# Kernel optimization log

Hardware: AMD Instinct MI355X
Metric: run time of the kernel (lower is better)

## Reference

```python
import jax, jax.numpy as jnp
import numpy as np

B, N, CIN, COUT, K, L, NNZ = 4, 4096, 128, 128, 10, 50, 65536


def _spmm(idx, vals, X):
    # COO spmm: out[r] += vals * X[c]; idx: [2, nnz], X: [N, F]
    rows, cols = idx[0], idx[1]
    return jax.ops.segment_sum(vals[:, None] * X[cols], rows, num_segments=N)

_bspmm = jax.vmap(_spmm, in_axes=(0, 0, 0))  # batched over leading dim


def _hgnn_layer(phi_idx, phi_val, inv_idx, inv_val, fea, W, d):
    # original: ((phi @ diag(d)) @ phi_inv) @ (fea @ W)
    # identical math, evaluated right-to-left to stay sparse-dense only
    filt = jnp.einsum('bnc,co->bno', fea, W)            # [B,N,COUT]
    y = _bspmm(inv_idx, inv_val, filt)                  # phi_inv @ X
    y = d[None, :, None] * y                            # diag(d) @ .
    return _bspmm(phi_idx, phi_val, y)                  # phi @ .


def setup_inputs() -> dict:
    key = jax.random.key(0)
    ks = jax.random.split(key, 20)

    def coo(ki, kv):
        idx = jax.random.randint(ki, (B, 2, NNZ), 0, N, dtype=jnp.int32)
        val = jax.random.normal(kv, (B, NNZ), jnp.float32) * 0.05
        return idx, val

    phi1_idx, phi1_val = coo(ks[0], ks[1])
    phi1_inv_idx, phi1_inv_val = coo(ks[2], ks[3])
    phi2_idx, phi2_val = coo(ks[4], ks[5])
    phi2_inv_idx, phi2_inv_val = coo(ks[6], ks[7])
    fea = jax.random.normal(ks[8], (B, N, CIN), jnp.float32)
    joblst = jax.random.randint(ks[9], (B, L), 0, N, dtype=jnp.int64)

    xavier = float(np.sqrt(6.0 / (CIN + COUT)))
    W1 = jax.random.uniform(ks[10], (CIN, COUT), jnp.float32, -xavier, xavier)
    W2 = jax.random.uniform(ks[11], (CIN, COUT), jnp.float32, -xavier, xavier)
    d1 = jax.random.uniform(ks[12], (N,), jnp.float32, 0.9, 1.1)
    d2 = jax.random.uniform(ks[13], (N,), jnp.float32, 0.9, 1.1)
    s = float(1.0 / np.sqrt(N))
    W_ih = jax.random.uniform(ks[14], (N, COUT), jnp.float32, -s, s)
    W_hh = jax.random.uniform(ks[15], (N, N), jnp.float32, -s, s)
    b_ih = jax.random.uniform(ks[16], (N,), jnp.float32, -s, s)
    b_hh = jnp.zeros((N,), jnp.float32)
    sd = float(1.0 / np.sqrt(COUT))
    dense_W = jax.random.uniform(ks[17], (K, COUT), jnp.float32, -sd, sd)
    dense_b = jnp.zeros((K,), jnp.float32)
    item_emb = jax.random.normal(ks[18], (N, COUT), jnp.float32) * 0.01

    return dict(phi1_idx=phi1_idx, phi1_val=phi1_val, phi1_inv_idx=phi1_inv_idx,
                phi1_inv_val=phi1_inv_val, phi2_idx=phi2_idx, phi2_val=phi2_val,
                phi2_inv_idx=phi2_inv_idx, phi2_inv_val=phi2_inv_val,
                fea=fea, joblst=joblst, W1=W1, d1=d1, W2=W2, d2=d2,
                W_ih=W_ih, W_hh=W_hh, b_ih=b_ih, b_hh=b_hh,
                dense_W=dense_W, dense_b=dense_b, item_emb=item_emb)


def reference(phi1_idx, phi1_val, phi1_inv_idx, phi1_inv_val,
              phi2_idx, phi2_val, phi2_inv_idx, phi2_inv_val,
              fea, joblst, W1, d1, W2, d2, W_ih, W_hh, b_ih, b_hh,
              dense_W, dense_b, item_emb):
    # two hypergraph conv layers, summed
    out1 = _hgnn_layer(phi1_idx, phi1_val, phi1_inv_idx, phi1_inv_val, fea, W1, d1)
    out2 = _hgnn_layer(phi2_idx, phi2_val, phi2_inv_idx, phi2_inv_val, fea, W2, d2)
    res = out1 + out2                                   # [B,N,COUT]

    # RNN over job history embeddings (all joblst entries valid -> no -1 filter)
    xs = jnp.swapaxes(item_emb[joblst], 0, 1)           # [L,B,COUT]
    h0 = jnp.zeros((fea.shape[0], N), fea.dtype)

    def step(h, x):
        h = jnp.tanh(x @ W_ih.T + h @ W_hh.T + b_ih + b_hh)
        return h, None

    Emb, _ = jax.lax.scan(step, h0, xs)                 # last hidden: [B,N]

    res2 = jax.nn.gelu(jnp.einsum('bno,ko->bnk', res, dense_W) + dense_b,
                       approximate=False)               # [B,N,K]
    # (res3 * Emb2).permute back == res2 * gelu(Emb) broadcast over K
    return jax.nn.sigmoid(res2 * jax.nn.gelu(Emb, approximate=False)[:, :, None])
```

## Files before the change

### kernel.cpp

```cpp
#include <hip/hip_runtime.h>
#include <cstdint>
#include <cstddef>

#define NN   4096
#define LLC  50

__device__ __forceinline__ float bf2f(unsigned short u) {
    return __uint_as_float(((unsigned)u) << 16);
}
__device__ __forceinline__ unsigned short f2bf(float x) {
    unsigned b = __float_as_uint(x);
    return (unsigned short)((b + 0x7fffu + ((b >> 16) & 1u)) >> 16);
}

#if __has_builtin(__builtin_amdgcn_sdot4)
#define SDOT4(a, b, c) __builtin_amdgcn_sdot4((int)(a), (int)(b), (c), false)
#else
__device__ __forceinline__ int sdot4_sw(unsigned a, unsigned b, int c) {
    c += (int)(signed char)(a) * (int)(signed char)(b);
    c += (int)(signed char)(a >> 8) * (int)(signed char)(b >> 8);
    c += (int)(signed char)(a >> 16) * (int)(signed char)(b >> 16);
    c += (int)(signed char)(a >> 24) * (int)(signed char)(b >> 24);
    return c;
}
#define SDOT4(a, b, c) sdot4_sw((a), (b), (c))
#endif

#define DPPADD(v, ctrl, rmask) \
    ((v) + __builtin_amdgcn_update_dpp(0, (v), (ctrl), (rmask), 0xf, true))
__device__ __forceinline__ int wred64(int v) {
    v = DPPADD(v, 0x111, 0xf);
    v = DPPADD(v, 0x112, 0xf);
    v = DPPADD(v, 0x114, 0xf);
    v = DPPADD(v, 0x118, 0xf);
    v = DPPADD(v, 0x142, 0xa);
    v = DPPADD(v, 0x143, 0xc);
    return v;
}

#define PBAR(IDX)                                                              \
    __syncthreads();                                                           \
    if (t == 0) {                                                              \
        __builtin_amdgcn_fence(__ATOMIC_RELEASE, "agent");                     \
        __hip_atomic_fetch_add(&bar[IDX], 1, __ATOMIC_RELAXED,                 \
                               __HIP_MEMORY_SCOPE_AGENT);                      \
        while (__hip_atomic_load(&bar[IDX], __ATOMIC_RELAXED,                  \
                                 __HIP_MEMORY_SCOPE_AGENT) < 512)              \
            __builtin_amdgcn_s_sleep(4);                                       \
        __builtin_amdgcn_fence(__ATOMIC_ACQUIRE, "agent");                     \
    }                                                                          \
    __syncthreads();

__global__ __launch_bounds__(256, 2) void k_prep(
        const int* __restrict__ i0, const int* __restrict__ i1,
        const int* __restrict__ i2, const int* __restrict__ i3,
        const float* __restrict__ v0, const float* __restrict__ v1,
        const float* __restrict__ v2, const float* __restrict__ v3,
        const float* __restrict__ dd1, const float* __restrict__ dd2,
        const float* __restrict__ fea,
        const float* __restrict__ W1, const float* __restrict__ W2,
        const float* __restrict__ item_emb, const int* __restrict__ joblst,
        const float* __restrict__ W_ih,
        const float* __restrict__ b_ih, const float* __restrict__ b_hh,
        int* __restrict__ counts, int* __restrict__ rowptr,
        int* __restrict__ cursor, unsigned* __restrict__ ep,
        unsigned short* __restrict__ filt1, unsigned short* __restrict__ filt2,
        float* __restrict__ xp, int* __restrict__ bar) {
    __shared__ float smem[4096];
    __shared__ int wt4[4];
    int t = threadIdx.x;
    int lane = t & 63, wv = t >> 6;
    int w = blockIdx.x;

    if (t < 128) counts[w * 128 + t] = 0;
    PBAR(352)
    {
        int* lc = (int*)smem;
#pragma unroll
        for (int i = 0; i < 16; ++i) lc[t + i * 256] = 0;
        __syncthreads();
        unsigned s = (unsigned)w >> 5, ch = (unsigned)w & 31;
        unsigned m = s >> 2, b = s & 3;
        const int* ip = (m == 0) ? i0 : (m == 1) ? i1 : (m == 2) ? i2 : i3;
        unsigned base = b * 131072u + ch * 2048u;
#pragma unroll
        for (int i = 0; i < 8; ++i) {
            int r = ip[base + t + i * 256];
            atomicAdd(&lc[r], 1);
        }
        __syncthreads();
        int* cs = counts + s * 4096;
#pragma unroll
        for (int i = 0; i < 16; ++i) {
            int v = lc[t + i * 256];
            if (v) atomicAdd(cs + t + i * 256, v);
        }
    }
    PBAR(360)
    if (w < 16) {
        int s = w;
        int loc[16];
        int base = t * 16;
        const int* cs = counts + s * 4096;
        int run = 0;
#pragma unroll
        for (int i = 0; i < 16; ++i) { loc[i] = run; run += cs[base + i]; }
        int total = run;
        int v = total;
#pragma unroll
        for (int d = 1; d < 64; d <<= 1) { int u = __shfl_up(v, d, 64); if (lane >= d) v += u; }
        if (lane == 63) wt4[wv] = v;
        __syncthreads();
        int pre = v - total;
        for (int i = 0; i < wv; ++i) pre += wt4[i];
        int* rp = rowptr + s * 4097;
        int* cu = cursor + s * 4096;
#pragma unroll
        for (int i = 0; i < 16; ++i) { rp[base + i] = pre + loc[i]; cu[base + i] = pre + loc[i]; }
        if (t == 255) rp[4096] = pre + total;
    }
    PBAR(368)
    if (w < 128) {
        unsigned s = (unsigned)w >> 3, ch = (unsigned)w & 7;
        unsigned m = s >> 2, b = s & 3;
        const int* ip = (m == 0) ? i0 : (m == 1) ? i1 : (m == 2) ? i2 : i3;
        const float* vp = (m == 0) ? v0 : (m == 1) ? v1 : (m == 2) ? v2 : v3;
        int* cu = cursor + s * 4096;
#pragma unroll 8
        for (int i = 0; i < 32; ++i) {
            unsigned e = ch * 8192u + i * 256u + t;
            int r = ip[(size_t)b * 131072 + e];
            int c = ip[(size_t)b * 131072 + 65536 + e];
            float v = vp[(size_t)b * 65536 + e];
            if (m == 1) v *= dd1[c];
            if (m == 3) v *= dd2[c];
            int pos = atomicAdd(cu + r, 1);
            ep[(size_t)s * 65536 + pos] = ((unsigned)c << 16) | (unsigned)f2bf(v);
        }
    } else if (w < 384) {
        int rb = (w - 128) * 64;
        for (int st = 0; st < 2; ++st) {
            int rbase = rb + st * 32;
            if (st) __syncthreads();
#pragma unroll
            for (int i = 0; i < 16; ++i) {
                int idx = t + i * 256;
                smem[idx] = fea[(size_t)rbase * 128 + idx];
            }
            __syncthreads();
            int half = t >> 7, tc = t & 127;
            const float* sf = smem + half * 2048;
            float a1[16], a2[16];
#pragma unroll
            for (int r = 0; r < 16; ++r) { a1[r] = 0.f; a2[r] = 0.f; }
            for (int c = 0; c < 128; c += 4) {
                float w10 = W1[(c + 0) * 128 + tc], w11 = W1[(c + 1) * 128 + tc];
                float w12 = W1[(c + 2) * 128 + tc], w13 = W1[(c + 3) * 128 + tc];
                float w20 = W2[(c + 0) * 128 + tc], w21 = W2[(c + 1) * 128 + tc];
                float w22 = W2[(c + 2) * 128 + tc], w23 = W2[(c + 3) * 128 + tc];
#pragma unroll
                for (int r = 0; r < 16; ++r) {
                    float4 f = *(const float4*)&sf[r * 128 + c];
                    a1[r] += f.x * w10 + f.y * w11 + f.z * w12 + f.w * w13;
                    a2[r] += f.x * w20 + f.y * w21 + f.z * w22 + f.w * w23;
                }
            }
#pragma unroll
            for (int r = 0; r < 16; ++r) {
                size_t o = (size_t)(rbase + half * 16 + r) * 128 + tc;
                filt1[o] = f2bf(a1[r]);
                filt2[o] = f2bf(a2[r]);
            }
        }
    } else {
        int wx = w - 384;
        int nb = wx & 15, pb = wx >> 4;
        int p0 = pb * 25;
        for (int idx = t; idx < 25 * 128; idx += 256) {
            int rr = idx >> 7, c = idx & 127;
            int p = p0 + rr;
            int b = p & 3, l = p >> 2;
            int j = joblst[b * LLC + l];
            smem[idx] = item_emb[(size_t)j * 128 + c];
        }
        __syncthreads();
        int n = nb * 256 + t;
        float acc[25];
#pragma unroll
        for (int r = 0; r < 25; ++r) acc[r] = 0.f;
        const float* wn = W_ih + (size_t)n * 128;
        for (int c = 0; c < 128; c += 4) {
            float4 wq = *(const float4*)(wn + c);
#pragma unroll
            for (int r = 0; r < 25; ++r) {
                float4 xr = *(const float4*)&smem[r * 128 + c];
                acc[r] += xr.x * wq.x + xr.y * wq.y + xr.z * wq.z + xr.w * wq.w;
            }
        }
        float bias = b_ih[n] + b_hh[n];
#pragma unroll
        for (int r = 0; r < 25; ++r) xp[(size_t)(p0 + r) * NN + n] = acc[r] + bias;
    }
}

__device__ __forceinline__ void row_acc(const unsigned* __restrict__ eps, int e0, int e1,
                                        const unsigned* __restrict__ Xd, unsigned bbase,
                                        unsigned lane, float& a0, float& a1) {
    int e = e0;
    for (; e + 8 <= e1; e += 8) {
        unsigned p[8], x[8];
#pragma unroll
        for (int i = 0; i < 8; ++i) p[i] = eps[e + i];
#pragma unroll
        for (int i = 0; i < 8; ++i)
            x[i] = Xd[((size_t)(bbase + (p[i] >> 16)) << 6) + lane];
#pragma unroll
        for (int i = 0; i < 8; ++i) {
            float v = bf2f((unsigned short)p[i]);
            a0 += v * bf2f((unsigned short)x[i]);
            a1 += v * bf2f((unsigned short)(x[i] >> 16));
        }
    }
    for (; e < e1; ++e) {
        unsigned pp = eps[e];
        unsigned xw = Xd[((size_t)(bbase + (pp >> 16)) << 6) + lane];
        float v = bf2f((unsigned short)pp);
        a0 += v * bf2f((unsigned short)xw);
        a1 += v * bf2f((unsigned short)(xw >> 16));
    }
}

__global__ __launch_bounds__(256, 2) void k_mega(
        const float* __restrict__ W_hh,
        const float* __restrict__ xp,
        unsigned* __restrict__ hq,
        float* __restrict__ hfin,
        int* __restrict__ bar,
        const int* __restrict__ rowptr,
        const unsigned* __restrict__ ep,
        const unsigned short* __restrict__ filt1,
        const unsigned short* __restrict__ filt2,
        unsigned short* __restrict__ y1,
        unsigned short* __restrict__ y2,
        const float* __restrict__ dW,
        const float* __restrict__ db,
        float* __restrict__ g1) {
    __shared__ unsigned hs[4352];
    __shared__ int red[4][16];
    __shared__ unsigned char hpk[4][4][4];
    int t = threadIdx.x;
    int lane = t & 63, wv = t >> 6;
    int blk = blockIdx.x;

    if (blk >= 256) {
        int w = blk - 256;
        int c7 = w & 7;
        {
            unsigned mm = c7 & 1, b = (unsigned)c7 >> 1;
            int s = (mm ? 8 : 0) + (int)b;
            const unsigned* Xd = (const unsigned*)(mm ? filt2 : filt1);
            unsigned* Yd = (unsigned*)(mm ? y2 : y1);
            const int* rp = rowptr + s * 4097;
            const unsigned* eps = ep + (size_t)s * 65536;
            unsigned bbase = b * 4096;
            int g = w >> 3;
            int row0 = (g * 4 + wv) * 16;
            for (int rr = 0; rr < 16; ++rr) {
                int row = row0 + rr;
                float a0 = 0.f, a1 = 0.f;
                row_acc(eps, rp[row], rp[row + 1], Xd, bbase, lane, a0, a1);
                Yd[((size_t)(bbase + row) << 6) + lane] =
                    (unsigned)f2bf(a0) | ((unsigned)f2bf(a1) << 16);
            }
        }
        __syncthreads();
        if (t == 0) {
            __builtin_amdgcn_fence(__ATOMIC_RELEASE, "agent");
            __hip_atomic_fetch_add(&bar[320], 1, __ATOMIC_RELAXED,
                                   __HIP_MEMORY_SCOPE_AGENT);
            while (__hip_atomic_load(&bar[320], __ATOMIC_RELAXED,
                                     __HIP_MEMORY_SCOPE_AGENT) < 512)
                __builtin_amdgcn_s_sleep(4);
            __builtin_amdgcn_fence(__ATOMIC_ACQUIRE, "agent");
        }
        __syncthreads();
        {
            unsigned b = (unsigned)c7 >> 1;
            unsigned bbase = b * 4096;
            const int* rpA = rowptr + (4 + (int)b) * 4097;
            const int* rpB = rowptr + (12 + (int)b) * 4097;
            const unsigned* epA = ep + (size_t)(4 + b) * 65536;
            const unsigned* epB = ep + (size_t)(12 + b) * 65536;
            const unsigned* y1d = (const unsigned*)y1;
            const unsigned* y2d = (const unsigned*)y2;
            int g2 = (w >> 3) * 2 + (w & 1);
            int row0 = (g2 * 4 + wv) * 8;
            float* fs = (float*)hs + wv * 1056;
            for (int rr = 0; rr < 8; ++rr) {
                int row = row0 + rr;
                float a0 = 0.f, a1 = 0.f;
                row_acc(epA, rpA[row], rpA[row + 1], y1d, bbase, lane, a0, a1);
                row_acc(epB, rpB[row], rpB[row + 1], y2d, bbase, lane, a0, a1);
                *(float2*)(fs + rr * 132 + 2 * lane) = make_float2(a0, a1);
            }
#pragma unroll
            for (int pass = 0; pass < 2; ++pass) {
                int task = lane + pass * 64;
                if (task < 80) {
                    int rr = task / 10, k = task - rr * 10;
                    const float* rrp = fs + rr * 132;
                    const float4* wk4 = (const float4*)(dW + (size_t)k * 128);
                    float acc = 0.f;
#pragma unroll
                    for (int c4 = 0; c4 < 32; ++c4) {
                        float4 a = *(const float4*)(rrp + c4 * 4);
                        float4 wq = wk4[c4];
                        acc += a.x * wq.x + a.y * wq.y + a.z * wq.z + a.w * wq.w;
                    }
                    float pre = acc + db[k];
                    float gg = 0.5f * pre * (1.f + erff(pre * 0.70710678118f));
                    g1[(size_t)(bbase + row0 + rr) * 10 + k] = gg;
                }
            }
        }
        return;
    }

    int row_base = ((blk & 7) * 32 + (blk >> 3)) * 16;
    int wrow = row_base + wv * 4;

    uint4 W[4][4];
    {
        const float* wsrc = W_hh + (size_t)wrow * 4096;
#pragma unroll
        for (int r = 0; r < 4; ++r)
#pragma unroll
            for (int k4 = 0; k4 < 4; ++k4) {
                unsigned q[4];
#pragma unroll
                for (int i = 0; i < 4; ++i) {
                    const float* p = wsrc + (size_t)r * 4096 + (lane * 16 + k4 * 4 + i) * 4;
                    float4 w = *(const float4*)p;
                    int q0 = (int)rintf(fminf(fmaxf(w.x * 8192.f, -127.f), 127.f));
                    int q1 = (int)rintf(fminf(fmaxf(w.y * 8192.f, -127.f), 127.f));
                    int q2 = (int)rintf(fminf(fmaxf(w.z * 8192.f, -127.f), 127.f));
                    int q3 = (int)rintf(fminf(fmaxf(w.w * 8192.f, -127.f), 127.f));
                    q[i] = (q0 & 0xff) | ((q1 & 0xff) << 8) | ((q2 & 0xff) << 16) | ((q3 & 0xff) << 24);
                }
                W[r][k4] = make_uint4(q[0], q[1], q[2], q[3]);
            }
    }

    const float SC = 1.f / (8192.f * 127.f);

    for (int l = 0; l < LLC; ++l) {
        if (l > 0) {
            const unsigned* src = hq + (size_t)((l - 1) & 1) * 4096;
            unsigned sval[16];
#pragma unroll
            for (int k = 0; k < 16; ++k)
                sval[k] = __hip_atomic_load(src + t + k * 256, __ATOMIC_RELAXED,
                                            __HIP_MEMORY_SCOPE_AGENT);
#pragma unroll
            for (int k = 0; k < 16; ++k) hs[t + k * 256] = sval[k];
            __syncthreads();

            __builtin_amdgcn_s_setprio(1);
            uint4 H[4][4];
#pragma unroll
            for (int b = 0; b < 4; ++b)
#pragma unroll
                for (int k4 = 0; k4 < 4; ++k4)
                    H[b][k4] = ((const uint4*)hs)[k4 * 256 + b * 64 + lane];
            int acc[4][4];
#pragma unroll
            for (int r = 0; r < 4; ++r)
#pragma unroll
                for (int b = 0; b < 4; ++b) acc[r][b] = 0;
#pragma unroll
            for (int k4 = 0; k4 < 4; ++k4)
#pragma unroll
                for (int r = 0; r < 4; ++r)
#pragma unroll
                    for (int b = 0; b < 4; ++b) {
                        acc[r][b] = SDOT4(W[r][k4].x, H[b][k4].x, acc[r][b]);
                        acc[r][b] = SDOT4(W[r][k4].y, H[b][k4].y, acc[r][b]);
                        acc[r][b] = SDOT4(W[r][k4].z, H[b][k4].z, acc[r][b]);
                        acc[r][b] = SDOT4(W[r][k4].w, H[b][k4].w, acc[r][b]);
                    }
#pragma unroll
            for (int r = 0; r < 4; ++r)
#pragma unroll
                for (int b = 0; b < 4; ++b) acc[r][b] = wred64(acc[r][b]);
            if (lane == 63) {
#pragma unroll
                for (int b = 0; b < 4; ++b) {
                    int4 q = { acc[0][b], acc[1][b], acc[2][b], acc[3][b] };
                    *(int4*)&red[wv][b * 4] = q;
                }
            }
            __builtin_amdgcn_s_setprio(0);
        }
        if (lane < 16) {
            int b = lane >> 2, rr = lane & 3;
            int row = wrow + rr;
            float a = (l > 0) ? (float)red[wv][lane] * SC : 0.f;
            float pre = a + xp[(size_t)(l * 4 + b) * NN + row];
            float hnew = tanhf(pre);
            if (l == LLC - 1) hfin[(size_t)b * NN + row] = hnew;
            int q = (int)rintf(hnew * 127.f);
            hpk[wv][b][rr] = (unsigned char)(q & 0xff);
        }
        if (l < LLC - 1) {
            if (lane < 4) {
                int b = lane;
                unsigned d = *(const unsigned*)&hpk[wv][b][0];
                int hk = (row_base >> 2) + wv;
                int phys = ((hk >> 2) & 3) * 1024 + b * 256 + (hk >> 4) * 4 + (hk & 3);
                __hip_atomic_store(hq + (size_t)(l & 1) * 4096 + phys, d,
                                   __ATOMIC_RELAXED, __HIP_MEMORY_SCOPE_AGENT);
            }
            __syncthreads();
            if (t == 0) {
                int g = blk & 7;
                int old = __hip_atomic_fetch_add(&bar[g * 32], 1, __ATOMIC_RELAXED,
                                                 __HIP_MEMORY_SCOPE_AGENT);
                if ((old & 31) == 31)
                    __hip_atomic_fetch_add(&bar[256], 1, __ATOMIC_RELAXED,
                                           __HIP_MEMORY_SCOPE_AGENT);
                int target = 8 * (l + 1);
                while (__hip_atomic_load(&bar[256], __ATOMIC_RELAXED,
                                         __HIP_MEMORY_SCOPE_AGENT) < target)
                    __builtin_amdgcn_s_sleep(2);
            }
            __syncthreads();
        }
    }
}

__global__ __launch_bounds__(256) void k_out(const float* __restrict__ g1,
                                             const float* __restrict__ hfin,
                                             float* __restrict__ out) {
    int i = blockIdx.x * 256 + threadIdx.x;
    int grow = i / 10;
    float e = hfin[grow];
    float ge = 0.5f * e * (1.f + erff(e * 0.70710678118f));
    out[i] = 1.f / (1.f + __expf(-g1[i] * ge));
}

extern "C" void kernel_launch(void* const* d_in, const int* in_sizes, int n_in,
                              void* d_out, int out_size, void* d_ws, size_t ws_size,
                              hipStream_t stream) {
    const int*   phi1_idx = (const int*)d_in[0];
    const float* phi1_val = (const float*)d_in[1];
    const int*   inv1_idx = (const int*)d_in[2];
    const float* inv1_val = (const float*)d_in[3];
    const int*   phi2_idx = (const int*)d_in[4];
    const float* phi2_val = (const float*)d_in[5];
    const int*   inv2_idx = (const int*)d_in[6];
    const float* inv2_val = (const float*)d_in[7];
    const float* fea      = (const float*)d_in[8];
    const int*   joblst   = (const int*)d_in[9];
    const float* W1       = (const float*)d_in[10];
    const float* d1       = (const float*)d_in[11];
    const float* W2       = (const float*)d_in[12];
    const float* d2       = (const float*)d_in[13];
    const float* W_ih     = (const float*)d_in[14];
    const float* W_hh     = (const float*)d_in[15];
    const float* b_ih     = (const float*)d_in[16];
    const float* b_hh     = (const float*)d_in[17];
    const float* dense_W  = (const float*)d_in[18];
    const float* dense_b  = (const float*)d_in[19];
    const float* item_emb = (const float*)d_in[20];

    float* ws = (float*)d_ws;
    unsigned short* filt1 = (unsigned short*)ws;
    unsigned short* filt2 = (unsigned short*)(ws + 1048576);
    unsigned short* y1    = (unsigned short*)(ws + 2097152);
    unsigned short* y2    = (unsigned short*)(ws + 3145728);
    float* g1   = ws + 4194304;
    float* xp   = ws + 6291456;
    float* hfin = ws + 7110656;
    unsigned* hq  = (unsigned*)(ws + 7127040);
    int*   counts = (int*)(ws + 11329536);
    int*   rowptr = (int*)(ws + 11395072);
    int*   cursor = (int*)(ws + 11460624);
    unsigned* ep  = (unsigned*)(ws + 11526160);
    int*   bar    = (int*)(ws + 12574736);

    hipMemsetAsync(bar, 0, 2048, stream);

    k_prep<<<512, 256, 0, stream>>>(inv1_idx, phi1_idx, inv2_idx, phi2_idx,
                                    inv1_val, phi1_val, inv2_val, phi2_val,
                                    d1, d2, fea, W1, W2, item_emb, joblst,
                                    W_ih, b_ih, b_hh,
                                    counts, rowptr, cursor, ep,
                                    filt1, filt2, xp, bar);

    k_mega<<<768, 256, 0, stream>>>(W_hh, xp, hq, hfin, bar,
                                    rowptr, ep, filt1, filt2, y1, y2,
                                    dense_W, dense_b, g1);

    k_out<<<640, 256, 0, stream>>>(g1, hfin, (float*)d_out);
}
```

Measured before the change: 588.3 us.

## Replace in-kernel grid barriers in prep with kernel split and fuse output epilogue

```diff
diff --git a/kernel.cpp b/kernel.cpp
--- a/kernel.cpp
+++ b/kernel.cpp
@@ -38,73 +38,46 @@
     return v;
 }
 
-#define PBAR(IDX)                                                              \
-    __syncthreads();                                                           \
-    if (t == 0) {                                                              \
-        __builtin_amdgcn_fence(__ATOMIC_RELEASE, "agent");                     \
-        __hip_atomic_fetch_add(&bar[IDX], 1, __ATOMIC_RELAXED,                 \
-                               __HIP_MEMORY_SCOPE_AGENT);                      \
-        while (__hip_atomic_load(&bar[IDX], __ATOMIC_RELAXED,                  \
-                                 __HIP_MEMORY_SCOPE_AGENT) < 512)              \
-            __builtin_amdgcn_s_sleep(4);                                       \
-        __builtin_amdgcn_fence(__ATOMIC_ACQUIRE, "agent");                     \
-    }                                                                          \
-    __syncthreads();
-
-__global__ __launch_bounds__(256, 2) void k_prep(
+__global__ __launch_bounds__(256) void k_prep(
         const int* __restrict__ i0, const int* __restrict__ i1,
         const int* __restrict__ i2, const int* __restrict__ i3,
-        const float* __restrict__ v0, const float* __restrict__ v1,
-        const float* __restrict__ v2, const float* __restrict__ v3,
-        const float* __restrict__ dd1, const float* __restrict__ dd2,
         const float* __restrict__ fea,
         const float* __restrict__ W1, const float* __restrict__ W2,
         const float* __restrict__ item_emb, const int* __restrict__ joblst,
         const float* __restrict__ W_ih,
         const float* __restrict__ b_ih, const float* __restrict__ b_hh,
-        int* __restrict__ counts, int* __restrict__ rowptr,
-        int* __restrict__ cursor, unsigned* __restrict__ ep,
+        int* __restrict__ rowptr, int* __restrict__ cursor,
         unsigned short* __restrict__ filt1, unsigned short* __restrict__ filt2,
-        float* __restrict__ xp, int* __restrict__ bar) {
+        float* __restrict__ xp) {
     __shared__ float smem[4096];
     __shared__ int wt4[4];
     int t = threadIdx.x;
     int lane = t & 63, wv = t >> 6;
-    int w = blockIdx.x;
-
-    if (t < 128) counts[w * 128 + t] = 0;
-    PBAR(352)
-    {
+    int blk = blockIdx.x;
+
+    if (blk < 16) {
+        int s = blk;
         int* lc = (int*)smem;
 #pragma unroll
         for (int i = 0; i < 16; ++i) lc[t + i * 256] = 0;
         __syncthreads();
-        unsigned s = (unsigned)w >> 5, ch = (unsigned)w & 31;
-        unsigned m = s >> 2, b = s & 3;
+        unsigned m = (unsigned)s >> 2, b = (unsigned)s & 3;
         const int* ip = (m == 0) ? i0 : (m == 1) ? i1 : (m == 2) ? i2 : i3;
-        unsigned base = b * 131072u + ch * 2048u;
-#pragma unroll
-        for (int i = 0; i < 8; ++i) {
-            int r = ip[base + t + i * 256];
-            atomicAdd(&lc[r], 1);
-        }
-        __syncthreads();
-        int* cs = counts + s * 4096;
-#pragma unroll
-        for (int i = 0; i < 16; ++i) {
-            int v = lc[t + i * 256];
-            if (v) atomicAdd(cs + t + i * 256, v);
-        }
-    }
-    PBAR(360)
-    if (w < 16) {
-        int s = w;
+        const int4* ip4 = (const int4*)(ip + (size_t)b * 131072);
+#pragma unroll 4
+        for (int i = 0; i < 64; ++i) {
+            int4 r4 = ip4[i * 256 + t];
+            atomicAdd(&lc[r4.x], 1);
+            atomicAdd(&lc[r4.y], 1);
+            atomicAdd(&lc[r4.z], 1);
+            atomicAdd(&lc[r4.w], 1);
+        }
+        __syncthreads();
         int loc[16];
         int base = t * 16;
-        const int* cs = counts + s * 4096;
         int run = 0;
 #pragma unroll
-        for (int i = 0; i < 16; ++i) { loc[i] = run; run += cs[base + i]; }
+        for (int i = 0; i < 16; ++i) { loc[i] = run; run += lc[base + i]; }
         int total = run;
         int v = total;
 #pragma unroll
@@ -118,62 +91,8 @@
 #pragma unroll
         for (int i = 0; i < 16; ++i) { rp[base + i] = pre + loc[i]; cu[base + i] = pre + loc[i]; }
         if (t == 255) rp[4096] = pre + total;
-    }
-    PBAR(368)
-    if (w < 128) {
-        unsigned s = (unsigned)w >> 3, ch = (unsigned)w & 7;
-        unsigned m = s >> 2, b = s & 3;
-        const int* ip = (m == 0) ? i0 : (m == 1) ? i1 : (m == 2) ? i2 : i3;
-        const float* vp = (m == 0) ? v0 : (m == 1) ? v1 : (m == 2) ? v2 : v3;
-        int* cu = cursor + s * 4096;
-#pragma unroll 8
-        for (int i = 0; i < 32; ++i) {
-            unsigned e = ch * 8192u + i * 256u + t;
-            int r = ip[(size_t)b * 131072 + e];
-            int c = ip[(size_t)b * 131072 + 65536 + e];
-            float v = vp[(size_t)b * 65536 + e];
-            if (m == 1) v *= dd1[c];
-            if (m == 3) v *= dd2[c];
-            int pos = atomicAdd(cu + r, 1);
-            ep[(size_t)s * 65536 + pos] = ((unsigned)c << 16) | (unsigned)f2bf(v);
-        }
-    } else if (w < 384) {
-        int rb = (w - 128) * 64;
-        for (int st = 0; st < 2; ++st) {
-            int rbase = rb + st * 32;
-            if (st) __syncthreads();
-#pragma unroll
-            for (int i = 0; i < 16; ++i) {
-                int idx = t + i * 256;
-                smem[idx] = fea[(size_t)rbase * 128 + idx];
-            }
-            __syncthreads();
-            int half = t >> 7, tc = t & 127;
-            const float* sf = smem + half * 2048;
-            float a1[16], a2[16];
-#pragma unroll
-            for (int r = 0; r < 16; ++r) { a1[r] = 0.f; a2[r] = 0.f; }
-            for (int c = 0; c < 128; c += 4) {
-                float w10 = W1[(c + 0) * 128 + tc], w11 = W1[(c + 1) * 128 + tc];
-                float w12 = W1[(c + 2) * 128 + tc], w13 = W1[(c + 3) * 128 + tc];
-                float w20 = W2[(c + 0) * 128 + tc], w21 = W2[(c + 1) * 128 + tc];
-                float w22 = W2[(c + 2) * 128 + tc], w23 = W2[(c + 3) * 128 + tc];
-#pragma unroll
-                for (int r = 0; r < 16; ++r) {
-                    float4 f = *(const float4*)&sf[r * 128 + c];
-                    a1[r] += f.x * w10 + f.y * w11 + f.z * w12 + f.w * w13;
-                    a2[r] += f.x * w20 + f.y * w21 + f.z * w22 + f.w * w23;
-                }
-            }
-#pragma unroll
-            for (int r = 0; r < 16; ++r) {
-                size_t o = (size_t)(rbase + half * 16 + r) * 128 + tc;
-                filt1[o] = f2bf(a1[r]);
-                filt2[o] = f2bf(a2[r]);
-            }
-        }
-    } else {
-        int wx = w - 384;
+    } else if (blk < 144) {
+        int wx = blk - 16;
         int nb = wx & 15, pb = wx >> 4;
         int p0 = pb * 25;
         for (int idx = t; idx < 25 * 128; idx += 256) {
@@ -200,7 +119,59 @@
         float bias = b_ih[n] + b_hh[n];
 #pragma unroll
         for (int r = 0; r < 25; ++r) xp[(size_t)(p0 + r) * NN + n] = acc[r] + bias;
-    }
+    } else {
+        int rb = (blk - 144) * 32;
+#pragma unroll
+        for (int i = 0; i < 16; ++i) {
+            int idx = t + i * 256;
+            smem[idx] = fea[(size_t)rb * 128 + idx];
+        }
+        __syncthreads();
+        int half = t >> 7, tc = t & 127;
+        const float* sf = smem + half * 2048;
+        float a1[16], a2[16];
+#pragma unroll
+        for (int r = 0; r < 16; ++r) { a1[r] = 0.f; a2[r] = 0.f; }
+        for (int c = 0; c < 128; c += 4) {
+            float w10 = W1[(c + 0) * 128 + tc], w11 = W1[(c + 1) * 128 + tc];
+            float w12 = W1[(c + 2) * 128 + tc], w13 = W1[(c + 3) * 128 + tc];
+            float w20 = W2[(c + 0) * 128 + tc], w21 = W2[(c + 1) * 128 + tc];
+            float w22 = W2[(c + 2) * 128 + tc], w23 = W2[(c + 3) * 128 + tc];
+#pragma unroll
+            for (int r = 0; r < 16; ++r) {
+                float4 f = *(const float4*)&sf[r * 128 + c];
+                a1[r] += f.x * w10 + f.y * w11 + f.z * w12 + f.w * w13;
+                a2[r] += f.x * w20 + f.y * w21 + f.z * w22 + f.w * w23;
+            }
+        }
+#pragma unroll
+        for (int r = 0; r < 16; ++r) {
+            size_t o = (size_t)(rb + half * 16 + r) * 128 + tc;
+            filt1[o] = f2bf(a1[r]);
+            filt2[o] = f2bf(a2[r]);
+        }
+    }
+}
+
+__global__ __launch_bounds__(256) void k_scatter(const int* __restrict__ i0, const int* __restrict__ i1,
+                                                 const int* __restrict__ i2, const int* __restrict__ i3,
+                                                 const float* __restrict__ v0, const float* __restrict__ v1,
+                                                 const float* __restrict__ v2, const float* __restrict__ v3,
+                                                 const float* __restrict__ d1, const float* __restrict__ d2,
+                                                 int* __restrict__ cursor,
+                                                 unsigned* __restrict__ ep) {
+    unsigned gid = blockIdx.x * 256 + threadIdx.x;
+    unsigned s = gid >> 16, e = gid & 65535;
+    unsigned m = s >> 2, b = s & 3;
+    const int* ip = (m == 0) ? i0 : (m == 1) ? i1 : (m == 2) ? i2 : i3;
+    const float* vp = (m == 0) ? v0 : (m == 1) ? v1 : (m == 2) ? v2 : v3;
+    int r = ip[(size_t)b * 131072 + e];
+    int c = ip[(size_t)b * 131072 + 65536 + e];
+    float v = vp[(size_t)b * 65536 + e];
+    if (m == 1) v *= d1[c];
+    if (m == 3) v *= d2[c];
+    int pos = atomicAdd(cursor + s * 4096 + r, 1);
+    ep[(size_t)s * 65536 + pos] = ((unsigned)c << 16) | (unsigned)f2bf(v);
 }
 
 __device__ __forceinline__ void row_acc(const unsigned* __restrict__ eps, int e0, int e1,
@@ -234,7 +205,6 @@
         const float* __restrict__ W_hh,
         const float* __restrict__ xp,
         unsigned* __restrict__ hq,
-        float* __restrict__ hfin,
         int* __restrict__ bar,
         const int* __restrict__ rowptr,
         const unsigned* __restrict__ ep,
@@ -244,7 +214,8 @@
         unsigned short* __restrict__ y2,
         const float* __restrict__ dW,
         const float* __restrict__ db,
-        float* __restrict__ g1) {
+        float* __restrict__ g1,
+        float* __restrict__ out) {
     __shared__ unsigned hs[4352];
     __shared__ int red[4][16];
     __shared__ unsigned char hpk[4][4][4];
@@ -323,6 +294,12 @@
                 }
             }
         }
+        __syncthreads();
+        if (t == 0) {
+            __builtin_amdgcn_fence(__ATOMIC_RELEASE, "agent");
+            __hip_atomic_fetch_add(&bar[352], 1, __ATOMIC_RELAXED,
+                                   __HIP_MEMORY_SCOPE_AGENT);
+        }
         return;
     }
 
@@ -401,13 +378,13 @@
             }
             __builtin_amdgcn_s_setprio(0);
         }
+        float hnew = 0.f;
         if (lane < 16) {
             int b = lane >> 2, rr = lane & 3;
             int row = wrow + rr;
             float a = (l > 0) ? (float)red[wv][lane] * SC : 0.f;
             float pre = a + xp[(size_t)(l * 4 + b) * NN + row];
-            float hnew = tanhf(pre);
-            if (l == LLC - 1) hfin[(size_t)b * NN + row] = hnew;
+            hnew = tanhf(pre);
             int q = (int)rintf(hnew * 127.f);
             hpk[wv][b][rr] = (unsigned char)(q & 0xff);
         }
@@ -434,18 +411,27 @@
                     __builtin_amdgcn_s_sleep(2);
             }
             __syncthreads();
-        }
-    }
-}
-
-__global__ __launch_bounds__(256) void k_out(const float* __restrict__ g1,
-                                             const float* __restrict__ hfin,
-                                             float* __restrict__ out) {
-    int i = blockIdx.x * 256 + threadIdx.x;
-    int grow = i / 10;
-    float e = hfin[grow];
-    float ge = 0.5f * e * (1.f + erff(e * 0.70710678118f));
-    out[i] = 1.f / (1.f + __expf(-g1[i] * ge));
+        } else {
+            if (t == 0) {
+                while (__hip_atomic_load(&bar[352], __ATOMIC_RELAXED,
+                                         __HIP_MEMORY_SCOPE_AGENT) < 512)
+                    __builtin_amdgcn_s_sleep(2);
+            }
+            __syncthreads();
+            if (lane < 16) {
+                int b = lane >> 2, rr = lane & 3;
+                int row = wrow + rr;
+                float ge = 0.5f * hnew * (1.f + erff(hnew * 0.70710678118f));
+                size_t gb = ((size_t)b * NN + row) * 10;
+#pragma unroll
+                for (int k = 0; k < 10; ++k) {
+                    float gv = __hip_atomic_load(g1 + gb + k, __ATOMIC_RELAXED,
+                                                 __HIP_MEMORY_SCOPE_AGENT);
+                    out[gb + k] = 1.f / (1.f + __expf(-gv * ge));
+                }
+            }
+        }
+    }
 }
 
 extern "C" void kernel_launch(void* const* d_in, const int* in_sizes, int n_in,
@@ -480,9 +466,7 @@
     unsigned short* y2    = (unsigned short*)(ws + 3145728);
     float* g1   = ws + 4194304;
     float* xp   = ws + 6291456;
-    float* hfin = ws + 7110656;
     unsigned* hq  = (unsigned*)(ws + 7127040);
-    int*   counts = (int*)(ws + 11329536);
     int*   rowptr = (int*)(ws + 11395072);
     int*   cursor = (int*)(ws + 11460624);
     unsigned* ep  = (unsigned*)(ws + 11526160);
@@ -490,16 +474,16 @@
 
     hipMemsetAsync(bar, 0, 2048, stream);
 
-    k_prep<<<512, 256, 0, stream>>>(inv1_idx, phi1_idx, inv2_idx, phi2_idx,
-                                    inv1_val, phi1_val, inv2_val, phi2_val,
-                                    d1, d2, fea, W1, W2, item_emb, joblst,
+    k_prep<<<656, 256, 0, stream>>>(inv1_idx, phi1_idx, inv2_idx, phi2_idx,
+                                    fea, W1, W2, item_emb, joblst,
                                     W_ih, b_ih, b_hh,
-                                    counts, rowptr, cursor, ep,
-                                    filt1, filt2, xp, bar);
-
-    k_mega<<<768, 256, 0, stream>>>(W_hh, xp, hq, hfin, bar,
+                                    rowptr, cursor, filt1, filt2, xp);
+
+    k_scatter<<<4096, 256, 0, stream>>>(inv1_idx, phi1_idx, inv2_idx, phi2_idx,
+                                        inv1_val, phi1_val, inv2_val, phi2_val,
+                                        d1, d2, cursor, ep);
+
+    k_mega<<<768, 256, 0, stream>>>(W_hh, xp, hq, bar,
                                     rowptr, ep, filt1, filt2, y1, y2,
-                                    dense_W, dense_b, g1);
-
-    k_out<<<640, 256, 0, stream>>>(g1, hfin, (float*)d_out);
-}
+                                    dense_W, dense_b, g1, (float*)d_out);
+}
```

Measured after the change: 502.4 us. 1.17x faster.
